# Optimization experiments

Measured on AMD Instinct MI355X. Metric: run time of the kernel, lower is better.

## Reference

```python
import jax, jax.numpy as jnp
import numpy as np

L, B, D = 50, 1024, 512      # memory slots, batch, d_model
H, DK = 4, 512               # heads, per-head dim (d_k = d_model in this module)
HOP = 3


def setup_inputs() -> dict:
    key = jax.random.key(0)
    ks = jax.random.split(key, 16)
    s = lambda i, shape: jax.random.normal(ks[i], shape, jnp.float32) * 0.02
    return dict(
        momery=jax.random.normal(ks[0], (L, B, D), jnp.float32),
        hid=jax.random.normal(ks[1], (B, D), jnp.float32),
        text_polarity=jax.random.normal(ks[2], (B,), jnp.float32),
        attribute_polarity=jax.random.normal(ks[3], (B,), jnp.float32),
        w=jnp.array(0.5, jnp.float32),
        p_w1=s(4, (D, D)), p_b1=jnp.zeros((D,), jnp.float32),
        p_w2=s(5, (D, D)), p_b2=jnp.zeros((D,), jnp.float32),
        wq=s(6, (D, H * DK)), bq=jnp.zeros((H * DK,), jnp.float32),
        wk=s(7, (D, H * DK)), bk=jnp.zeros((H * DK,), jnp.float32),
        wv=s(8, (D, H * DK)), bv=jnp.zeros((H * DK,), jnp.float32),
        wo=s(9, (H * DK, D)), bo=jnp.zeros((D,), jnp.float32),
    )


def reference(momery, hid, text_polarity, attribute_polarity, w,
              p_w1, p_b1, p_w2, p_b2, wq, bq, wk, bk, wv, bv, wo, bo):
    # k, v depend only on hid (attinkv = hid every hop/slot) -> hoist out of hop loop
    k = (hid @ wk + bk).reshape(B, H, DK)   # [B,H,DK]
    v = (hid @ wv + bv).reshape(B, H, DK)   # [B,H,DK]
    inv_sqrt_dk = jnp.float32(1.0 / np.sqrt(DK))
    for _ in range(HOP):
        # projection MLP over all slots at once (replaces per-slot loop)
        mid = jax.nn.relu(momery @ p_w1 + p_b1) @ p_w2 + p_b2          # [L,B,D]
        q = (mid @ wq + bq).reshape(L, B, H, DK)                        # [L,B,H,DK]
        # single key per query (nk=1): scores [L,B,H,1], softmax -> ones
        scores = (jnp.einsum('lbhd,bhd->lbh', q, k) * inv_sqrt_dk)[..., None]
        att = jax.nn.softmax(scores, axis=-1)                           # [L,B,H,1]
        out = att * v                                                   # [L,B,H,DK]
        temp = out.reshape(L, B, H * DK) @ wo + bo                      # [L,B,D]
        momery = momery + w * temp
    return momery
```

## Files before the change

### kernel.cpp

```cpp
#include <hip/hip_runtime.h>
#include <hip/hip_bf16.h>

#define B_SZ 1024
#define D_SZ 512

typedef short short8 __attribute__((ext_vector_type(8)));
typedef float f4 __attribute__((ext_vector_type(4)));

__device__ __forceinline__ short f2bfs(float f) {
    __hip_bfloat16 h = __float2bfloat16(f);
    return __builtin_bit_cast(short, h);
}

__global__ __launch_bounds__(256) void gemmA(const float* __restrict__ wv,
                                             const float* __restrict__ wo,
                                             const float* __restrict__ bv,
                                             const float* __restrict__ bo,
                                             float* __restrict__ Wp,
                                             float* __restrict__ b2p) {
    constexpr int K = 2048, N = 512, NT = 16;
    const int tid  = threadIdx.x;
    const int col0 = blockIdx.x * 64;
    const int row0 = blockIdx.y * 64;
    const int z    = blockIdx.z;
    const int k0   = z * 512;

    const int lane = tid & 63;
    const int wave = tid >> 6;
    const int mq = wave >> 1, nq = wave & 1;
    const int ln = lane & 15, q = lane >> 4;

    const int rowA0 = row0 + mq * 32 + ln;
    const int rowA1 = rowA0 + 16;
    const int colB0 = col0 + nq * 32 + ln;
    const int colB1 = colB0 + 16;

    const float* pa0 = wv + (size_t)rowA0 * K + k0 + q * 8;
    const float* pa1 = wv + (size_t)rowA1 * K + k0 + q * 8;
    const float* pb  = wo + (size_t)(k0 + q * 8) * N;

    float4 a00 = *(const float4*)pa0, a01 = *(const float4*)(pa0 + 4);
    float4 a10 = *(const float4*)pa1, a11 = *(const float4*)(pa1 + 4);
    float b0r[8], b1r[8];
#pragma unroll
    for (int j = 0; j < 8; ++j) {
        b0r[j] = pb[(size_t)j * N + colB0];
        b1r[j] = pb[(size_t)j * N + colB1];
    }

    f4 acc00 = {0,0,0,0}, acc01 = {0,0,0,0}, acc10 = {0,0,0,0}, acc11 = {0,0,0,0};

    for (int t = 0; t < NT; ++t) {
        short8 af0, af1, bf0, bf1;
        af0[0]=f2bfs(a00.x); af0[1]=f2bfs(a00.y); af0[2]=f2bfs(a00.z); af0[3]=f2bfs(a00.w);
        af0[4]=f2bfs(a01.x); af0[5]=f2bfs(a01.y); af0[6]=f2bfs(a01.z); af0[7]=f2bfs(a01.w);
        af1[0]=f2bfs(a10.x); af1[1]=f2bfs(a10.y); af1[2]=f2bfs(a10.z); af1[3]=f2bfs(a10.w);
        af1[4]=f2bfs(a11.x); af1[5]=f2bfs(a11.y); af1[6]=f2bfs(a11.z); af1[7]=f2bfs(a11.w);
#pragma unroll
        for (int j = 0; j < 8; ++j) { bf0[j] = f2bfs(b0r[j]); bf1[j] = f2bfs(b1r[j]); }

        if (t + 1 < NT) {
            pa0 += 32; pa1 += 32; pb += (size_t)32 * N;
            a00 = *(const float4*)pa0; a01 = *(const float4*)(pa0 + 4);
            a10 = *(const float4*)pa1; a11 = *(const float4*)(pa1 + 4);
#pragma unroll
            for (int j = 0; j < 8; ++j) {
                b0r[j] = pb[(size_t)j * N + colB0];
                b1r[j] = pb[(size_t)j * N + colB1];
            }
        }
        acc00 = __builtin_amdgcn_mfma_f32_16x16x32_bf16(af0, bf0, acc00, 0, 0, 0);
        acc01 = __builtin_amdgcn_mfma_f32_16x16x32_bf16(af0, bf1, acc01, 0, 0, 0);
        acc10 = __builtin_amdgcn_mfma_f32_16x16x32_bf16(af1, bf0, acc10, 0, 0, 0);
        acc11 = __builtin_amdgcn_mfma_f32_16x16x32_bf16(af1, bf1, acc11, 0, 0, 0);
    }

    float* C = Wp + (size_t)z * 262144;
    const int r0 = row0 + mq * 32 + q * 4;
    const int c0 = col0 + nq * 32 + ln;
#pragma unroll
    for (int r = 0; r < 4; ++r) {
        C[(size_t)(r0 + r) * N + c0]           = acc00[r];
        C[(size_t)(r0 + r) * N + c0 + 16]      = acc01[r];
        C[(size_t)(r0 + 16 + r) * N + c0]      = acc10[r];
        C[(size_t)(r0 + 16 + r) * N + c0 + 16] = acc11[r];
    }

    if (z == 0) {
        int bid = blockIdx.y * 8 + blockIdx.x;
        int g = bid * 256 + tid;
        int o = g & 511;
        int r = g >> 9;
        float s = (r == 0) ? bo[o] : 0.f;
        int j0 = r * 64;
#pragma unroll 8
        for (int j = j0; j < j0 + 64; ++j) s += bv[j] * wo[j * 512 + o];
        b2p[r * 512 + o] = s;
    }
}

__global__ __launch_bounds__(256) void gemmB(const float* __restrict__ hid,
                                             const float* __restrict__ Wp,
                                             const float* __restrict__ b2p,
                                             float* __restrict__ t0,
                                             float* __restrict__ t1) {
    constexpr int K = 512, N = 512, NT = 8;
    __shared__ float biasS[64];

    const int tid  = threadIdx.x;
    const int col0 = blockIdx.x * 64;
    const int row0 = blockIdx.y * 64;
    const int z    = blockIdx.z;
    const int k0   = z * 256;

    const int lane = tid & 63;
    const int wave = tid >> 6;
    const int mq = wave >> 1, nq = wave & 1;
    const int ln = lane & 15, q = lane >> 4;

    const int rowA0 = row0 + mq * 32 + ln;
    const int rowA1 = rowA0 + 16;
    const int colB0 = col0 + nq * 32 + ln;
    const int colB1 = colB0 + 16;

    const float* pa0 = hid + (size_t)rowA0 * K + k0 + q * 8;
    const float* pa1 = hid + (size_t)rowA1 * K + k0 + q * 8;
    const float* pb  = Wp + (size_t)(k0 + q * 8) * N;

    float4 a00 = *(const float4*)pa0, a01 = *(const float4*)(pa0 + 4);
    float4 a10 = *(const float4*)pa1, a11 = *(const float4*)(pa1 + 4);
    float b0r[8], b1r[8];
#pragma unroll
    for (int j = 0; j < 8; ++j) {
        size_t off = (size_t)j * N;
        b0r[j] = pb[off + colB0]           + pb[off + colB0 + 262144]
               + pb[off + colB0 + 524288]  + pb[off + colB0 + 786432];
        b1r[j] = pb[off + colB1]           + pb[off + colB1 + 262144]
               + pb[off + colB1 + 524288]  + pb[off + colB1 + 786432];
    }

    f4 acc00 = {0,0,0,0}, acc01 = {0,0,0,0}, acc10 = {0,0,0,0}, acc11 = {0,0,0,0};

    for (int t = 0; t < NT; ++t) {
        short8 af0, af1, bf0, bf1;
        af0[0]=f2bfs(a00.x); af0[1]=f2bfs(a00.y); af0[2]=f2bfs(a00.z); af0[3]=f2bfs(a00.w);
        af0[4]=f2bfs(a01.x); af0[5]=f2bfs(a01.y); af0[6]=f2bfs(a01.z); af0[7]=f2bfs(a01.w);
        af1[0]=f2bfs(a10.x); af1[1]=f2bfs(a10.y); af1[2]=f2bfs(a10.z); af1[3]=f2bfs(a10.w);
        af1[4]=f2bfs(a11.x); af1[5]=f2bfs(a11.y); af1[6]=f2bfs(a11.z); af1[7]=f2bfs(a11.w);
#pragma unroll
        for (int j = 0; j < 8; ++j) { bf0[j] = f2bfs(b0r[j]); bf1[j] = f2bfs(b1r[j]); }

        if (t + 1 < NT) {
            pa0 += 32; pa1 += 32; pb += (size_t)32 * N;
            a00 = *(const float4*)pa0; a01 = *(const float4*)(pa0 + 4);
            a10 = *(const float4*)pa1; a11 = *(const float4*)(pa1 + 4);
#pragma unroll
            for (int j = 0; j < 8; ++j) {
                size_t off = (size_t)j * N;
                b0r[j] = pb[off + colB0]           + pb[off + colB0 + 262144]
                       + pb[off + colB0 + 524288]  + pb[off + colB0 + 786432];
                b1r[j] = pb[off + colB1]           + pb[off + colB1 + 262144]
                       + pb[off + colB1 + 524288]  + pb[off + colB1 + 786432];
            }
        }
        acc00 = __builtin_amdgcn_mfma_f32_16x16x32_bf16(af0, bf0, acc00, 0, 0, 0);
        acc01 = __builtin_amdgcn_mfma_f32_16x16x32_bf16(af0, bf1, acc01, 0, 0, 0);
        acc10 = __builtin_amdgcn_mfma_f32_16x16x32_bf16(af1, bf0, acc10, 0, 0, 0);
        acc11 = __builtin_amdgcn_mfma_f32_16x16x32_bf16(af1, bf1, acc11, 0, 0, 0);
    }

    if (z == 0 && tid < 64) {
        float s = 0.f;
#pragma unroll 8
        for (int r = 0; r < 32; ++r) s += b2p[r * 512 + col0 + tid];
        biasS[tid] = s;
    }
    __syncthreads();
    float bj0 = 0.f, bj1 = 0.f;
    if (z == 0) { bj0 = biasS[nq * 32 + ln]; bj1 = biasS[nq * 32 + 16 + ln]; }

    float* C = z ? t1 : t0;
    const int r0 = row0 + mq * 32 + q * 4;
    const int c0 = col0 + nq * 32 + ln;
#pragma unroll
    for (int r = 0; r < 4; ++r) {
        C[(size_t)(r0 + r) * N + c0]           = acc00[r] + bj0;
        C[(size_t)(r0 + r) * N + c0 + 16]      = acc01[r] + bj1;
        C[(size_t)(r0 + 16 + r) * N + c0]      = acc10[r] + bj0;
        C[(size_t)(r0 + 16 + r) * N + c0 + 16] = acc11[r] + bj1;
    }
}

__global__ __launch_bounds__(256) void bcast_add_kernel(const float* __restrict__ mem,
                                                        const float* __restrict__ t0,
                                                        const float* __restrict__ t1,
                                                        const float* __restrict__ wp,
                                                        float* __restrict__ out) {
    int idx = blockIdx.x * 256 + threadIdx.x;
    const float4 mv = ((const float4*)mem)[idx];
    int bd = idx & ((B_SZ * D_SZ / 4) - 1);
    const float4 a = ((const float4*)t0)[bd];
    const float4 b = ((const float4*)t1)[bd];
    float s = 3.0f * wp[0];
    float4 o;
    o.x = mv.x + s * (a.x + b.x);
    o.y = mv.y + s * (a.y + b.y);
    o.z = mv.z + s * (a.z + b.z);
    o.w = mv.w + s * (a.w + b.w);
    ((float4*)out)[idx] = o;
}

extern "C" void kernel_launch(void* const* d_in, const int* in_sizes, int n_in,
                              void* d_out, int out_size, void* d_ws, size_t ws_size,
                              hipStream_t stream) {
    const float* momery = (const float*)d_in[0];
    const float* hid    = (const float*)d_in[1];
    const float* w      = (const float*)d_in[4];
    const float* wv     = (const float*)d_in[13];
    const float* bv     = (const float*)d_in[14];
    const float* wo     = (const float*)d_in[15];
    const float* bo     = (const float*)d_in[16];
    float* out = (float*)d_out;

    float* Wp  = (float*)d_ws;
    float* b2p = Wp + 4 * 262144;
    float* t0  = b2p + 16384;
    float* t1  = t0 + 524288;

    gemmA<<<dim3(8, 8, 4), 256, 0, stream>>>(wv, wo, bv, bo, Wp, b2p);

    gemmB<<<dim3(8, 16, 2), 256, 0, stream>>>(hid, Wp, b2p, t0, t1);

    bcast_add_kernel<<<25600, 256, 0, stream>>>(momery, t0, t1, w, out);
}
```

Before: 251.2 us.

## Fuse second GEMM with broadcast memory add and store pre-scaled bf16 transposed weight

The weight-product GEMM now splits K across two wave halves inside one block and reduces them through shared memory. It writes a transposed bf16 weight already scaled by 3w, instead of four fp32 partial slices. The hid GEMM and the broadcast add over the 50 memory slots are fused into one kernel, so the t0/t1 intermediates are never written and read back, and one launch is removed. The trade-off is fewer blocks for the weight GEMM (64 large blocks) and a long serial per-block loop streaming memory, which may lower occupancy and memory-level parallelism.

```diff
diff --git a/kernel.cpp b/kernel.cpp
--- a/kernel.cpp
+++ b/kernel.cpp
@@ -1,8 +1,5 @@
 #include <hip/hip_runtime.h>
 #include <hip/hip_bf16.h>
-
-#define B_SZ 1024
-#define D_SZ 512
 
 typedef short short8 __attribute__((ext_vector_type(8)));
 typedef float f4 __attribute__((ext_vector_type(4)));
@@ -12,23 +9,50 @@
     return __builtin_bit_cast(short, h);
 }
 
-__global__ __launch_bounds__(256) void gemmA(const float* __restrict__ wv,
+__device__ __forceinline__ unsigned packbf2(float a, float b, float s) {
+    unsigned lo = (unsigned short)f2bfs(s * a);
+    unsigned hi = (unsigned short)f2bfs(s * b);
+    return (hi << 16) | lo;
+}
+
+__device__ __forceinline__ float4 add4(float4 m, float4 t) {
+    float4 o; o.x = m.x + t.x; o.y = m.y + t.y; o.z = m.z + t.z; o.w = m.w + t.w;
+    return o;
+}
+
+__global__ __launch_bounds__(512) void prepW(const float* __restrict__ wv,
                                              const float* __restrict__ wo,
                                              const float* __restrict__ bv,
-                                             const float* __restrict__ bo,
-                                             float* __restrict__ Wp,
+                                             const float* __restrict__ w,
+                                             short* __restrict__ WsT,
                                              float* __restrict__ b2p) {
-    constexpr int K = 2048, N = 512, NT = 16;
-    const int tid  = threadIdx.x;
-    const int col0 = blockIdx.x * 64;
-    const int row0 = blockIdx.y * 64;
-    const int z    = blockIdx.z;
-    const int k0   = z * 512;
-
+    constexpr int K = 2048, N = 512, NT = 32;
+    const int tid = threadIdx.x;
+    const int bx  = blockIdx.x;
+
+    if (bx >= 64) {
+        const int jb  = bx - 64;
+        const int col = tid;
+        const float* pv = bv + jb * 512;
+        const float* pw = wo + (size_t)(jb * 512) * N + col;
+        float s = 0.f;
+#pragma unroll 8
+        for (int j = 0; j < 512; ++j) s += pv[j] * pw[(size_t)j * N];
+        b2p[jb * 512 + col] = s;
+        return;
+    }
+
+    __shared__ float red[64][65];
+
+    const int col0 = (bx & 7) * 64;
+    const int row0 = (bx >> 3) * 64;
     const int lane = tid & 63;
     const int wave = tid >> 6;
-    const int mq = wave >> 1, nq = wave & 1;
+    const int half = wave >> 2;
+    const int wq   = wave & 3;
+    const int mq = wq >> 1, nq = wq & 1;
     const int ln = lane & 15, q = lane >> 4;
+    const int k0 = half * 1024;
 
     const int rowA0 = row0 + mq * 32 + ln;
     const int rowA1 = rowA0 + 16;
@@ -75,139 +99,112 @@
         acc11 = __builtin_amdgcn_mfma_f32_16x16x32_bf16(af1, bf1, acc11, 0, 0, 0);
     }
 
-    float* C = Wp + (size_t)z * 262144;
-    const int r0 = row0 + mq * 32 + q * 4;
-    const int c0 = col0 + nq * 32 + ln;
-#pragma unroll
-    for (int r = 0; r < 4; ++r) {
-        C[(size_t)(r0 + r) * N + c0]           = acc00[r];
-        C[(size_t)(r0 + r) * N + c0 + 16]      = acc01[r];
-        C[(size_t)(r0 + 16 + r) * N + c0]      = acc10[r];
-        C[(size_t)(r0 + 16 + r) * N + c0 + 16] = acc11[r];
-    }
-
-    if (z == 0) {
-        int bid = blockIdx.y * 8 + blockIdx.x;
-        int g = bid * 256 + tid;
-        int o = g & 511;
-        int r = g >> 9;
-        float s = (r == 0) ? bo[o] : 0.f;
-        int j0 = r * 64;
-#pragma unroll 8
-        for (int j = j0; j < j0 + 64; ++j) s += bv[j] * wo[j * 512 + o];
-        b2p[r * 512 + o] = s;
-    }
-}
-
-__global__ __launch_bounds__(256) void gemmB(const float* __restrict__ hid,
-                                             const float* __restrict__ Wp,
-                                             const float* __restrict__ b2p,
-                                             float* __restrict__ t0,
-                                             float* __restrict__ t1) {
-    constexpr int K = 512, N = 512, NT = 8;
-    __shared__ float biasS[64];
+    const int lr0 = mq * 32 + q * 4;
+    const int lc0 = nq * 32 + ln;
+
+    if (half == 1) {
+#pragma unroll
+        for (int r = 0; r < 4; ++r) {
+            red[lr0 + r][lc0]           = acc00[r];
+            red[lr0 + r][lc0 + 16]      = acc01[r];
+            red[lr0 + 16 + r][lc0]      = acc10[r];
+            red[lr0 + 16 + r][lc0 + 16] = acc11[r];
+        }
+    }
+    __syncthreads();
+    if (half == 0) {
+        const float wsc = 3.0f * w[0];
+#pragma unroll
+        for (int r = 0; r < 4; ++r) {
+            acc00[r] += red[lr0 + r][lc0];
+            acc01[r] += red[lr0 + r][lc0 + 16];
+            acc10[r] += red[lr0 + 16 + r][lc0];
+            acc11[r] += red[lr0 + 16 + r][lc0 + 16];
+        }
+        short* p0 = WsT + (size_t)(col0 + lc0) * 512 + row0 + lr0;
+        short* p1 = WsT + (size_t)(col0 + lc0 + 16) * 512 + row0 + lr0;
+        *(unsigned*)(p0)      = packbf2(acc00[0], acc00[1], wsc);
+        *(unsigned*)(p0 + 2)  = packbf2(acc00[2], acc00[3], wsc);
+        *(unsigned*)(p0 + 16) = packbf2(acc10[0], acc10[1], wsc);
+        *(unsigned*)(p0 + 18) = packbf2(acc10[2], acc10[3], wsc);
+        *(unsigned*)(p1)      = packbf2(acc01[0], acc01[1], wsc);
+        *(unsigned*)(p1 + 2)  = packbf2(acc01[2], acc01[3], wsc);
+        *(unsigned*)(p1 + 16) = packbf2(acc11[0], acc11[1], wsc);
+        *(unsigned*)(p1 + 18) = packbf2(acc11[2], acc11[3], wsc);
+    }
+}
+
+__global__ __launch_bounds__(256) void fusedTB(const float* __restrict__ hid,
+                                               const short* __restrict__ WsT,
+                                               const float* __restrict__ b2p,
+                                               const float* __restrict__ bo,
+                                               const float* __restrict__ w,
+                                               const float* __restrict__ mem,
+                                               float* __restrict__ out) {
+    constexpr int KD = 512, NT = 16;
+    constexpr size_t LS = 1024 * 512 / 4;
+    __shared__ float tT[16][64];
 
     const int tid  = threadIdx.x;
-    const int col0 = blockIdx.x * 64;
-    const int row0 = blockIdx.y * 64;
-    const int z    = blockIdx.z;
-    const int k0   = z * 256;
-
+    const int b0   = blockIdx.x * 16;
+    const int c0   = blockIdx.y * 64;
     const int lane = tid & 63;
     const int wave = tid >> 6;
-    const int mq = wave >> 1, nq = wave & 1;
     const int ln = lane & 15, q = lane >> 4;
-
-    const int rowA0 = row0 + mq * 32 + ln;
-    const int rowA1 = rowA0 + 16;
-    const int colB0 = col0 + nq * 32 + ln;
-    const int colB1 = colB0 + 16;
-
-    const float* pa0 = hid + (size_t)rowA0 * K + k0 + q * 8;
-    const float* pa1 = hid + (size_t)rowA1 * K + k0 + q * 8;
-    const float* pb  = Wp + (size_t)(k0 + q * 8) * N;
-
-    float4 a00 = *(const float4*)pa0, a01 = *(const float4*)(pa0 + 4);
-    float4 a10 = *(const float4*)pa1, a11 = *(const float4*)(pa1 + 4);
-    float b0r[8], b1r[8];
-#pragma unroll
-    for (int j = 0; j < 8; ++j) {
-        size_t off = (size_t)j * N;
-        b0r[j] = pb[off + colB0]           + pb[off + colB0 + 262144]
-               + pb[off + colB0 + 524288]  + pb[off + colB0 + 786432];
-        b1r[j] = pb[off + colB1]           + pb[off + colB1 + 262144]
-               + pb[off + colB1 + 524288]  + pb[off + colB1 + 786432];
-    }
-
-    f4 acc00 = {0,0,0,0}, acc01 = {0,0,0,0}, acc10 = {0,0,0,0}, acc11 = {0,0,0,0};
+    const int row = b0 + ln;
+    const int col = c0 + wave * 16 + ln;
+
+    const int sr  = tid >> 4;
+    const int sc4 = tid & 15;
+    const size_t sbase = (size_t)(b0 + sr) * 512 + c0 + sc4 * 4;
+    const float4* mp = (const float4*)(mem + sbase);
+    float4*       op = (float4*)(out + sbase);
+    float4 m0 = mp[0], m1 = mp[LS], m2 = mp[2 * LS], m3 = mp[3 * LS], m4 = mp[4 * LS];
+
+    const float* pa  = hid + (size_t)row * KD + q * 8;
+    const short* pbw = WsT + (size_t)col * KD + q * 8;
+
+    float4 a0 = *(const float4*)pa, a1 = *(const float4*)(pa + 4);
+    short8 bf = *(const short8*)pbw;
+    f4 acc = {0, 0, 0, 0};
 
     for (int t = 0; t < NT; ++t) {
-        short8 af0, af1, bf0, bf1;
-        af0[0]=f2bfs(a00.x); af0[1]=f2bfs(a00.y); af0[2]=f2bfs(a00.z); af0[3]=f2bfs(a00.w);
-        af0[4]=f2bfs(a01.x); af0[5]=f2bfs(a01.y); af0[6]=f2bfs(a01.z); af0[7]=f2bfs(a01.w);
-        af1[0]=f2bfs(a10.x); af1[1]=f2bfs(a10.y); af1[2]=f2bfs(a10.z); af1[3]=f2bfs(a10.w);
-        af1[4]=f2bfs(a11.x); af1[5]=f2bfs(a11.y); af1[6]=f2bfs(a11.z); af1[7]=f2bfs(a11.w);
-#pragma unroll
-        for (int j = 0; j < 8; ++j) { bf0[j] = f2bfs(b0r[j]); bf1[j] = f2bfs(b1r[j]); }
-
+        short8 af;
+        af[0]=f2bfs(a0.x); af[1]=f2bfs(a0.y); af[2]=f2bfs(a0.z); af[3]=f2bfs(a0.w);
+        af[4]=f2bfs(a1.x); af[5]=f2bfs(a1.y); af[6]=f2bfs(a1.z); af[7]=f2bfs(a1.w);
+        short8 bc = bf;
         if (t + 1 < NT) {
-            pa0 += 32; pa1 += 32; pb += (size_t)32 * N;
-            a00 = *(const float4*)pa0; a01 = *(const float4*)(pa0 + 4);
-            a10 = *(const float4*)pa1; a11 = *(const float4*)(pa1 + 4);
-#pragma unroll
-            for (int j = 0; j < 8; ++j) {
-                size_t off = (size_t)j * N;
-                b0r[j] = pb[off + colB0]           + pb[off + colB0 + 262144]
-                       + pb[off + colB0 + 524288]  + pb[off + colB0 + 786432];
-                b1r[j] = pb[off + colB1]           + pb[off + colB1 + 262144]
-                       + pb[off + colB1 + 524288]  + pb[off + colB1 + 786432];
-            }
-        }
-        acc00 = __builtin_amdgcn_mfma_f32_16x16x32_bf16(af0, bf0, acc00, 0, 0, 0);
-        acc01 = __builtin_amdgcn_mfma_f32_16x16x32_bf16(af0, bf1, acc01, 0, 0, 0);
-        acc10 = __builtin_amdgcn_mfma_f32_16x16x32_bf16(af1, bf0, acc10, 0, 0, 0);
-        acc11 = __builtin_amdgcn_mfma_f32_16x16x32_bf16(af1, bf1, acc11, 0, 0, 0);
-    }
-
-    if (z == 0 && tid < 64) {
-        float s = 0.f;
-#pragma unroll 8
-        for (int r = 0; r < 32; ++r) s += b2p[r * 512 + col0 + tid];
-        biasS[tid] = s;
-    }
+            pa += 32; pbw += 32;
+            a0 = *(const float4*)pa; a1 = *(const float4*)(pa + 4);
+            bf = *(const short8*)pbw;
+        }
+        acc = __builtin_amdgcn_mfma_f32_16x16x32_bf16(af, bc, acc, 0, 0, 0);
+    }
+
+    const float wsc  = 3.0f * w[0];
+    const float bias = wsc * (b2p[col] + b2p[512 + col] + b2p[1024 + col] +
+                              b2p[1536 + col] + bo[col]);
+#pragma unroll
+    for (int r = 0; r < 4; ++r) tT[q * 4 + r][wave * 16 + ln] = acc[r] + bias;
     __syncthreads();
-    float bj0 = 0.f, bj1 = 0.f;
-    if (z == 0) { bj0 = biasS[nq * 32 + ln]; bj1 = biasS[nq * 32 + 16 + ln]; }
-
-    float* C = z ? t1 : t0;
-    const int r0 = row0 + mq * 32 + q * 4;
-    const int c0 = col0 + nq * 32 + ln;
-#pragma unroll
-    for (int r = 0; r < 4; ++r) {
-        C[(size_t)(r0 + r) * N + c0]           = acc00[r] + bj0;
-        C[(size_t)(r0 + r) * N + c0 + 16]      = acc01[r] + bj1;
-        C[(size_t)(r0 + 16 + r) * N + c0]      = acc10[r] + bj0;
-        C[(size_t)(r0 + 16 + r) * N + c0 + 16] = acc11[r] + bj1;
-    }
-}
-
-__global__ __launch_bounds__(256) void bcast_add_kernel(const float* __restrict__ mem,
-                                                        const float* __restrict__ t0,
-                                                        const float* __restrict__ t1,
-                                                        const float* __restrict__ wp,
-                                                        float* __restrict__ out) {
-    int idx = blockIdx.x * 256 + threadIdx.x;
-    const float4 mv = ((const float4*)mem)[idx];
-    int bd = idx & ((B_SZ * D_SZ / 4) - 1);
-    const float4 a = ((const float4*)t0)[bd];
-    const float4 b = ((const float4*)t1)[bd];
-    float s = 3.0f * wp[0];
-    float4 o;
-    o.x = mv.x + s * (a.x + b.x);
-    o.y = mv.y + s * (a.y + b.y);
-    o.z = mv.z + s * (a.z + b.z);
-    o.w = mv.w + s * (a.w + b.w);
-    ((float4*)out)[idx] = o;
+
+    const float4 tv = *(const float4*)&tT[sr][sc4 * 4];
+
+    op[0]      = add4(m0, tv);
+    op[LS]     = add4(m1, tv);
+    op[2 * LS] = add4(m2, tv);
+    op[3 * LS] = add4(m3, tv);
+    op[4 * LS] = add4(m4, tv);
+    mp += 5 * LS; op += 5 * LS;
+    for (int c = 1; c < 10; ++c) {
+        m0 = mp[0]; m1 = mp[LS]; m2 = mp[2 * LS]; m3 = mp[3 * LS]; m4 = mp[4 * LS];
+        op[0]      = add4(m0, tv);
+        op[LS]     = add4(m1, tv);
+        op[2 * LS] = add4(m2, tv);
+        op[3 * LS] = add4(m3, tv);
+        op[4 * LS] = add4(m4, tv);
+        mp += 5 * LS; op += 5 * LS;
+    }
 }
 
 extern "C" void kernel_launch(void* const* d_in, const int* in_sizes, int n_in,
@@ -222,14 +219,10 @@
     const float* bo     = (const float*)d_in[16];
     float* out = (float*)d_out;
 
-    float* Wp  = (float*)d_ws;
-    float* b2p = Wp + 4 * 262144;
-    float* t0  = b2p + 16384;
-    float* t1  = t0 + 524288;
-
-    gemmA<<<dim3(8, 8, 4), 256, 0, stream>>>(wv, wo, bv, bo, Wp, b2p);
-
-    gemmB<<<dim3(8, 16, 2), 256, 0, stream>>>(hid, Wp, b2p, t0, t1);
-
-    bcast_add_kernel<<<25600, 256, 0, stream>>>(momery, t0, t1, w, out);
-}
+    short* WsT = (short*)d_ws;
+    float* b2p = (float*)(WsT + 262144);
+
+    prepW<<<dim3(68), 512, 0, stream>>>(wv, wo, bv, w, WsT, b2p);
+
+    fusedTB<<<dim3(64, 8), 256, 0, stream>>>(hid, WsT, b2p, bo, w, momery, out);
+}
```

Measured after the change: 275.8 us. +9.8%, slower.
